# Optimization experiments

Measured on AMD Instinct MI355X. Metric: run time of the kernel, lower is better.

## Reference

```python
import jax, jax.numpy as jnp
import numpy as np

B, L, D_NODE, D_EDGE, H = 4, 256, 256, 128, 8
DK = D_NODE // H        # 32, per-head node dim
DE = D_EDGE // H        # 16, per-head edge dim
NEG_SLOPE = 0.2

# Static index maps replicating the torch loop indexing (including its j-1 off-by-one / wraparound bug)
_GIDX = np.arange(L - 1)[None, :] + (np.arange(L - 1)[None, :] >= np.arange(L)[:, None])  # [L, L-1]: j-values visited for row i (j != i, in order)
_PIDX = (np.arange(L) - 1) % (L - 1)   # [L]: torch uses attention_probs[:, j-1] for every j != i
_II = np.arange(L)[:, None]            # [L, 1]


def lrelu(x):
    return jnp.where(x >= 0, x, NEG_SLOPE * x)


def setup_inputs() -> dict:
    key = jax.random.key(0)
    ks = jax.random.split(key, 19)
    w = lambda k, s, sc=0.05: jax.random.normal(k, s, jnp.float32) * sc
    return dict(
        node=w(ks[0], (B, L, D_NODE), 1.0),
        edge=w(ks[1], (B, L, L, D_EDGE), 1.0),
        Wn_w=w(ks[2], (D_NODE, D_NODE)), Wn_b=w(ks[3], (D_NODE,)),
        Wh_w=w(ks[4], (DK, DK)), Wh_b=w(ks[5], (DK,)),
        We_w=w(ks[6], (D_EDGE, D_EDGE)), We_b=w(ks[7], (D_EDGE,)),
        Wn2_w=w(ks[8], (D_NODE, D_NODE)), Wn2_b=w(ks[9], (D_NODE,)),
        We2_w=w(ks[10], (D_EDGE, D_EDGE)), We2_b=w(ks[11], (D_EDGE,)),
        attn_w=w(ks[12], (2 * DK + DE,)),                  # attn_linear (no bias), input order [hi, hj, eij]
        edge_w=w(ks[13], (DE + 2 * DK, DE)), edge_b=w(ks[14], (DE,)),  # edge_linear, input order [eij, hi, hj]
        out_n_w=w(ks[15], (D_NODE, D_NODE)), out_n_b=w(ks[16], (D_NODE,)),
        out_e_w=w(ks[17], (D_EDGE, D_EDGE)), out_e_b=w(ks[18], (D_EDGE,)),
    )


def reference(node, edge, Wn_w, Wn_b, Wh_w, Wh_b, We_w, We_b, Wn2_w, Wn2_b,
              We2_w, We2_b, attn_w, edge_w, edge_b, out_n_w, out_n_b, out_e_w, out_e_b):
    node_p = (node @ Wn_w + Wn_b).reshape(B, L, H, DK)
    edge_p = (edge @ We_w + We_b).reshape(B, L, L, H, DE)

    # ---- node update (all heads at once) ----
    wq, wk, we = attn_w[:DK], attn_w[DK:2 * DK], attn_w[2 * DK:]
    si = jnp.einsum('bihd,d->bih', node_p, wq)
    sj = jnp.einsum('bjhd,d->bjh', node_p, wk)
    se = jnp.einsum('bijhd,d->bijh', edge_p, we)
    scores = si[:, :, None, :] + sj[:, None, :, :] + se          # [B,L,L,H], score(i,j)
    sc = scores[:, _II, _GIDX, :]                                 # [B,L,L-1,H]: j != i, loop order
    probs = jax.nn.softmax(lrelu(sc), axis=2)                     # softmax over the L-1 neighbors
    probs_pair = probs[:, :, _PIDX, :]                            # [B,L,L,H]: replicate probs[:, j-1]
    mask = (1.0 - jnp.eye(L, dtype=node.dtype))[None, :, :, None]
    Whh = jnp.einsum('bjhd,de->bjhe', node_p, Wh_w) + Wh_b        # Wh(hj), bias inside the sum
    agg = jnp.einsum('bijh,bjhe->bihe', probs_pair * mask, Whh)
    node_h = (node_p + lrelu(agg)).reshape(B, L, D_NODE)          # concat heads == reshape
    new_node = node_h @ out_n_w + out_n_b

    # ---- edge update ----
    node_p2 = (new_node @ Wn2_w + Wn2_b).reshape(B, L, H, DK)
    edge_p2 = (edge @ We2_w + We2_b).reshape(B, L, L, H, DE)
    w_e, w_i, w_j = edge_w[:DE], edge_w[DE:DE + DK], edge_w[DE + DK:]
    e_new = (jnp.einsum('bijhd,de->bijhe', edge_p2, w_e)
             + jnp.einsum('bihd,de->bihe', node_p2, w_i)[:, :, None]
             + jnp.einsum('bjhd,de->bjhe', node_p2, w_j)[:, None]
             + edge_b)
    e_new = e_new * mask[..., None]                               # diagonal stays zero (zeros_like init)
    new_edge = e_new.reshape(B, L, L, D_EDGE) @ out_e_w + out_e_b
    return new_node, new_edge
```

## Files before the change

### kernel.cpp

```cpp
#include <hip/hip_runtime.h>

#define Bb 4
#define Ll 256
#define NEG 0.2f

typedef __attribute__((ext_vector_type(8))) short short8;
typedef __attribute__((ext_vector_type(4))) float f32x4;
typedef __attribute__((ext_vector_type(4))) unsigned uint4v;

__device__ __forceinline__ float lrelu(float x) { return x >= 0.f ? x : NEG * x; }

__device__ __forceinline__ short f2bf(float x) {
  unsigned u = __builtin_bit_cast(unsigned, x);
  unsigned r = (u + 0x7FFFu + ((u >> 16) & 1u)) >> 16;
  return (short)r;
}

__device__ __forceinline__ unsigned pack2bf(float e, float o) {
  unsigned ue = __builtin_bit_cast(unsigned, e);
  unsigned uo = __builtin_bit_cast(unsigned, o);
  return ((ue + 0x8000u) >> 16) | ((uo + 0x8000u) & 0xFFFF0000u);
}

__device__ __forceinline__ float bflo(unsigned u) {
  return __builtin_bit_cast(float, u << 16);
}
__device__ __forceinline__ float bfhi(unsigned u) {
  return __builtin_bit_cast(float, u & 0xFFFF0000u);
}

__global__ void prep_kernel(const float* We_w, const float* We_b, const float* attn_w,
                            const float* We2_w, const float* We2_b, const float* edge_w,
                            const float* edge_b, const float* out_e_w, const float* out_e_b,
                            short* Vbf, float* chg, float* c0g, short* Gt) {
  int blk = blockIdx.x;
  int t = threadIdx.x;
  if (blk < 128) {
    __shared__ float m2[128];
    int c = blk;
    int h = t >> 4, e = t & 15;
    float s = 0.f;
    for (int d = 0; d < 16; ++d) s += We2_w[c * 128 + h * 16 + d] * edge_w[d * 16 + e];
    m2[t] = s;
    __syncthreads();
    float g = 0.f;
    for (int f = 0; f < 128; ++f) g += m2[f] * out_e_w[f * 128 + t];
    Gt[t * 128 + c] = f2bf(g);
  } else {
    __shared__ float b2e[128];
    const float* we = attn_w + 64;
    for (int idx = t; idx < 1024; idx += 128) {
      int c = idx >> 3, h = idx & 7;
      float s = 0.f;
      for (int d = 0; d < 16; ++d) s += We_w[c * 128 + h * 16 + d] * we[d];
      Vbf[h * 128 + c] = f2bf(s);
      Vbf[(h + 8) * 128 + c] = 0;
    }
    if (t < 8) {
      float s = 0.f;
      for (int d = 0; d < 16; ++d) s += We_b[t * 16 + d] * we[d];
      chg[t] = s;
    }
    {
      int h = t >> 4, e = t & 15;
      float s = 0.f;
      for (int d = 0; d < 16; ++d) s += We2_b[h * 16 + d] * edge_w[d * 16 + e];
      b2e[t] = s + edge_b[e];
    }
    __syncthreads();
    float s = out_e_b[t];
    for (int f = 0; f < 128; ++f) s += b2e[f] * out_e_w[f * 128 + t];
    c0g[t] = s;
  }
}

__global__ __launch_bounds__(256, 2) void edge_t_kernel(
    const float* __restrict__ edge, const short* __restrict__ Gt,
    const short* __restrict__ Vbf, const float* __restrict__ chg,
    short* __restrict__ Tf, float* __restrict__ seg) {
  int t = threadIdx.x;
  int l = t & 63, wid = t >> 6;
  int wm = wid >> 1, wn = wid & 1;
  int lc = l & 15, lq = l >> 4;
  long row0 = (long)blockIdx.x * 128;

  short8 bv[4][4];
#pragma unroll
  for (int ks = 0; ks < 4; ++ks)
#pragma unroll
    for (int nf = 0; nf < 4; ++nf)
      bv[ks][nf] = *(const short8*)(Gt + (wn * 64 + nf * 16 + lc) * 128 + ks * 32 + lq * 8);

  short8 vb[4];
#pragma unroll
  for (int ks = 0; ks < 4; ++ks) vb[ks] = *(const short8*)(Vbf + lc * 128 + ks * 32 + lq * 8);

  f32x4 accT[4][4];
#pragma unroll
  for (int mf = 0; mf < 4; ++mf)
#pragma unroll
    for (int nf = 0; nf < 4; ++nf) accT[mf][nf] = (f32x4){0.f, 0.f, 0.f, 0.f};
  f32x4 accS[4];
#pragma unroll
  for (int mf = 0; mf < 4; ++mf) accS[mf] = (f32x4){0.f, 0.f, 0.f, 0.f};

#pragma unroll
  for (int ks = 0; ks < 4; ++ks) {
    short8 av[4];
#pragma unroll
    for (int mf = 0; mf < 4; ++mf) {
      const float* ap = edge + (row0 + wm * 64 + mf * 16 + lc) * 128 + ks * 32 + lq * 8;
      float4 f0 = *(const float4*)ap;
      float4 f1 = *(const float4*)(ap + 4);
      uint4v u;
      u.x = pack2bf(f0.x, f0.y);
      u.y = pack2bf(f0.z, f0.w);
      u.z = pack2bf(f1.x, f1.y);
      u.w = pack2bf(f1.z, f1.w);
      av[mf] = __builtin_bit_cast(short8, u);
    }
#pragma unroll
    for (int mf = 0; mf < 4; ++mf)
#pragma unroll
      for (int nf = 0; nf < 4; ++nf)
        accT[mf][nf] =
            __builtin_amdgcn_mfma_f32_16x16x32_bf16(bv[ks][nf], av[mf], accT[mf][nf], 0, 0, 0);
    if (wn == 0) {
#pragma unroll
      for (int mf = 0; mf < 4; ++mf)
        accS[mf] = __builtin_amdgcn_mfma_f32_16x16x32_bf16(vb[ks], av[mf], accS[mf], 0, 0, 0);
    }
  }

  short* tb = Tf + (long)blockIdx.x * 16384;
#pragma unroll
  for (int mf = 0; mf < 4; ++mf)
#pragma unroll
    for (int np = 0; np < 2; ++np) {
      f32x4 a0 = accT[mf][2 * np];
      f32x4 a1 = accT[mf][2 * np + 1];
      uint4v u;
      u.x = pack2bf(a0.x, a0.y);
      u.y = pack2bf(a0.z, a0.w);
      u.z = pack2bf(a1.x, a1.y);
      u.w = pack2bf(a1.z, a1.w);
      *(uint4v*)(tb + (mf * 2 + np) * 2048 + t * 8) = u;
    }

  if (wn == 0 && lq < 2) {
    f32x4 chv = *(const f32x4*)(chg + lq * 4);
    long slab = blockIdx.x >> 1;
    int off = (blockIdx.x & 1) * 128;
#pragma unroll
    for (int mf = 0; mf < 4; ++mf) {
      int lrow = off + wm * 64 + mf * 16 + lc;
      f32x4 v = accS[mf] + chv;
      *(f32x4*)(seg + slab * 2048 + lrow * 8 + lq * 4) = v;
    }
  }
}

__global__ __launch_bounds__(256) void node_in_fused(
    const float* __restrict__ node, const float* __restrict__ Wn_w,
    const float* __restrict__ Wn_b, const float* __restrict__ Wh_w,
    const float* __restrict__ Wh_b, const float* __restrict__ attn_w,
    float* __restrict__ node_p, float* __restrict__ Whh, float* __restrict__ si,
    float* __restrict__ sj) {
  __shared__ float a[4][256];
  __shared__ float np[4][256];
  int t = threadIdx.x;
  int row0 = blockIdx.x * 4;
  for (int q = t; q < 1024; q += 256) a[q >> 8][q & 255] = node[(long)row0 * 256 + q];
  __syncthreads();
  float acc[4];
  float bvv = Wn_b[t];
#pragma unroll
  for (int r = 0; r < 4; ++r) acc[r] = bvv;
  for (int k = 0; k < 256; ++k) {
    float w = Wn_w[k * 256 + t];
#pragma unroll
    for (int r = 0; r < 4; ++r) acc[r] += a[r][k] * w;
  }
#pragma unroll
  for (int r = 0; r < 4; ++r) {
    node_p[(long)(row0 + r) * 256 + t] = acc[r];
    np[r][t] = acc[r];
  }
  __syncthreads();
  int h = t >> 5, e = t & 31;
  float wb2 = Wh_b[e];
#pragma unroll
  for (int r = 0; r < 4; ++r) {
    float s = wb2;
    for (int d = 0; d < 32; ++d) s += np[r][h * 32 + d] * Wh_w[d * 32 + e];
    Whh[(long)(row0 + r) * 256 + t] = s;
  }
  if (t < 64) {
    int r = t >> 4, idx = t & 15, hh = idx & 7;
    const float* w = attn_w + (idx < 8 ? 0 : 32);
    float s = 0.f;
    for (int d = 0; d < 32; ++d) s += np[r][hh * 32 + d] * w[d];
    ((idx < 8) ? si : sj)[(long)(row0 + r) * 8 + hh] = s;
  }
}

__global__ __launch_bounds__(256) void attn_fused(
    const float* __restrict__ node_p, const float* __restrict__ Whh,
    const float* __restrict__ si, const float* __restrict__ sj,
    const float* __restrict__ seg, float* __restrict__ node_h) {
  __shared__ float sjl[2048];
  __shared__ float sel[2048];
  __shared__ float pl[2048];
  __shared__ float sil[8];
  int t = threadIdx.x, bi = blockIdx.x;
  int b = bi >> 8, i = bi & 255;
  for (int q = t; q < 2048; q += 256) sjl[q] = sj[(long)b * 2048 + q];
  for (int q = t; q < 2048; q += 256) sel[q] = seg[(long)bi * 2048 + q];
  if (t < 8) sil[t] = si[(long)bi * 8 + t];
  __syncthreads();

  int g = t >> 5, l32 = t & 31;
  float sc[8];
  float mx = -1e30f;
#pragma unroll
  for (int m = 0; m < 8; ++m) {
    int k = l32 + 32 * m;
    float v = -1e30f;
    if (k < 255) {
      int jj = k + (k >= i ? 1 : 0);
      v = sil[g] + sjl[jj * 8 + g] + sel[jj * 8 + g];
      v = lrelu(v);
    }
    sc[m] = v;
    mx = fmaxf(mx, v);
  }
#pragma unroll
  for (int d = 16; d >= 1; d >>= 1) mx = fmaxf(mx, __shfl_xor(mx, d));
  float sum = 0.f;
#pragma unroll
  for (int m = 0; m < 8; ++m) {
    int k = l32 + 32 * m;
    float e = (k < 255) ? __expf(sc[m] - mx) : 0.f;
    sc[m] = e;
    sum += e;
  }
#pragma unroll
  for (int d = 16; d >= 1; d >>= 1) sum += __shfl_xor(sum, d);
  float inv = 1.f / sum;
#pragma unroll
  for (int m = 0; m < 8; ++m) {
    int k = l32 + 32 * m;
    if (k < 255) pl[k * 8 + g] = sc[m] * inv;
  }
  __syncthreads();

  int h = g;
  const float* wb = Whh + (long)b * 65536 + t;
  float acc0 = 0.f, acc1 = 0.f;
#pragma unroll 8
  for (int j = 0; j < 256; j += 2) {
    int k0 = (j == 0) ? 254 : (j - 1);
    int k1 = j;
    float w0 = (j == i) ? 0.f : pl[k0 * 8 + h];
    float w1 = (j + 1 == i) ? 0.f : pl[k1 * 8 + h];
    acc0 += w0 * wb[(long)j * 256];
    acc1 += w1 * wb[(long)(j + 1) * 256];
  }
  float acc = acc0 + acc1;
  float np = node_p[(long)bi * 256 + t];
  node_h[(long)bi * 256 + t] = np + lrelu(acc);
}

__global__ __launch_bounds__(256) void attn_fallback(
    const float* __restrict__ node_p, const float* __restrict__ Whh,
    const float* __restrict__ si, const float* __restrict__ sj,
    const float* __restrict__ edge, const short* __restrict__ Vbf,
    const float* __restrict__ chg, float* __restrict__ node_h) {
  __shared__ float sjl[2048];
  __shared__ float sel[2048];
  __shared__ float pl[2048];
  __shared__ float sil[8];
  int t = threadIdx.x, bi = blockIdx.x;
  int b = bi >> 8, i = bi & 255;
  for (int q = t; q < 2048; q += 256) sjl[q] = sj[(long)b * 2048 + q];
  if (t < 8) sil[t] = si[(long)bi * 8 + t];
  {
    int l = t & 63, w = t >> 6;
    int lc = l & 15, lq = l >> 4;
    short8 vb[4];
#pragma unroll
    for (int ks = 0; ks < 4; ++ks) vb[ks] = *(const short8*)(Vbf + lc * 128 + ks * 32 + lq * 8);
    f32x4 acc[4];
#pragma unroll
    for (int mf = 0; mf < 4; ++mf) acc[mf] = (f32x4){0.f, 0.f, 0.f, 0.f};
#pragma unroll
    for (int mf = 0; mf < 4; ++mf) {
      int row = w * 64 + mf * 16 + lc;
#pragma unroll
      for (int ks = 0; ks < 4; ++ks) {
        const float* ap = edge + (long)bi * 32768 + row * 128 + ks * 32 + lq * 8;
        float4 f0 = *(const float4*)ap;
        float4 f1 = *(const float4*)(ap + 4);
        uint4v u;
        u.x = pack2bf(f0.x, f0.y);
        u.y = pack2bf(f0.z, f0.w);
        u.z = pack2bf(f1.x, f1.y);
        u.w = pack2bf(f1.z, f1.w);
        acc[mf] = __builtin_amdgcn_mfma_f32_16x16x32_bf16(vb[ks], __builtin_bit_cast(short8, u),
                                                          acc[mf], 0, 0, 0);
      }
    }
    if (lq < 2) {
      f32x4 chv = *(const f32x4*)(chg + lq * 4);
#pragma unroll
      for (int mf = 0; mf < 4; ++mf) {
        int row = w * 64 + mf * 16 + lc;
        f32x4 v = acc[mf] + chv;
        *(f32x4*)(&sel[row * 8 + lq * 4]) = v;
      }
    }
  }
  __syncthreads();
  int g = t >> 5, l32 = t & 31;
  float sc[8];
  float mx = -1e30f;
#pragma unroll
  for (int m = 0; m < 8; ++m) {
    int k = l32 + 32 * m;
    float v = -1e30f;
    if (k < 255) {
      int jj = k + (k >= i ? 1 : 0);
      v = sil[g] + sjl[jj * 8 + g] + sel[jj * 8 + g];
      v = lrelu(v);
    }
    sc[m] = v;
    mx = fmaxf(mx, v);
  }
#pragma unroll
  for (int d = 16; d >= 1; d >>= 1) mx = fmaxf(mx, __shfl_xor(mx, d));
  float sum = 0.f;
#pragma unroll
  for (int m = 0; m < 8; ++m) {
    int k = l32 + 32 * m;
    float e = (k < 255) ? __expf(sc[m] - mx) : 0.f;
    sc[m] = e;
    sum += e;
  }
#pragma unroll
  for (int d = 16; d >= 1; d >>= 1) sum += __shfl_xor(sum, d);
  float inv = 1.f / sum;
#pragma unroll
  for (int m = 0; m < 8; ++m) {
    int k = l32 + 32 * m;
    if (k < 255) pl[k * 8 + g] = sc[m] * inv;
  }
  __syncthreads();
  int h = g;
  const float* wb = Whh + (long)b * 65536 + t;
  float acc0 = 0.f, acc1 = 0.f;
#pragma unroll 8
  for (int j = 0; j < 256; j += 2) {
    int k0 = (j == 0) ? 254 : (j - 1);
    int k1 = j;
    float w0 = (j == i) ? 0.f : pl[k0 * 8 + h];
    float w1 = (j + 1 == i) ? 0.f : pl[k1 * 8 + h];
    acc0 += w0 * wb[(long)j * 256];
    acc1 += w1 * wb[(long)(j + 1) * 256];
  }
  float acc = acc0 + acc1;
  float np = node_p[(long)bi * 256 + t];
  node_h[(long)bi * 256 + t] = np + lrelu(acc);
}

__global__ __launch_bounds__(256) void node_out_pq(
    const float* __restrict__ node_h, const float* __restrict__ out_n_w,
    const float* __restrict__ out_n_b, const float* __restrict__ Wn2_w,
    const float* __restrict__ Wn2_b, const float* __restrict__ edge_w,
    const float* __restrict__ out_e_w, float* __restrict__ out_node,
    float* __restrict__ Pg, float* __restrict__ Qg) {
  __shared__ float a[4][256];
  __shared__ float b2[4][256];
  __shared__ float ninj[4][256];
  int t = threadIdx.x;
  int row0 = blockIdx.x * 4;
  for (int q = t; q < 1024; q += 256) a[q >> 8][q & 255] = node_h[(long)row0 * 256 + q];
  __syncthreads();
  float acc[4];
  float bv1 = out_n_b[t];
#pragma unroll
  for (int r = 0; r < 4; ++r) acc[r] = bv1;
  for (int k = 0; k < 256; ++k) {
    float w = out_n_w[k * 256 + t];
#pragma unroll
    for (int r = 0; r < 4; ++r) acc[r] += a[r][k] * w;
  }
#pragma unroll
  for (int r = 0; r < 4; ++r) {
    out_node[(long)(row0 + r) * 256 + t] = acc[r];
    b2[r][t] = acc[r];
  }
  __syncthreads();
  float acc2[4];
  float bv2 = Wn2_b[t];
#pragma unroll
  for (int r = 0; r < 4; ++r) acc2[r] = bv2;
  for (int k = 0; k < 256; ++k) {
    float w = Wn2_w[k * 256 + t];
#pragma unroll
    for (int r = 0; r < 4; ++r) acc2[r] += b2[r][k] * w;
  }
#pragma unroll
  for (int r = 0; r < 4; ++r) a[r][t] = acc2[r];
  __syncthreads();
  {
    int f = t & 127, h = f >> 4, e = f & 15;
    const float* w = edge_w + 256 + (t >> 7) * 512;
#pragma unroll
    for (int r = 0; r < 4; ++r) {
      float s = 0.f;
      for (int d = 0; d < 32; ++d) s += a[r][h * 32 + d] * w[d * 16 + e];
      ninj[r][t] = s;
    }
  }
  __syncthreads();
  {
    int o = t & 127;
    int half = (t >> 7) * 128;
#pragma unroll
    for (int r = 0; r < 4; ++r) {
      float s = 0.f;
      const float* src = ninj[r] + half;
      for (int f = 0; f < 128; ++f) s += src[f] * out_e_w[f * 128 + o];
      ((t < 128) ? Pg : Qg)[(long)(row0 + r) * 128 + o] = s;
    }
  }
}

__global__ __launch_bounds__(256) void edge_final_kernel(
    const short* __restrict__ Tf, const float* __restrict__ Pg,
    const float* __restrict__ Qg, const float* __restrict__ c0g,
    const float* __restrict__ oeb, float* __restrict__ out_edge) {
  int t = threadIdx.x;
  int l = t & 63, wid = t >> 6;
  int wm = wid >> 1, wn = wid & 1;
  int lc = l & 15, lq = l >> 4;
  long row0 = (long)blockIdx.x * 128;
  int b = (int)(row0 >> 16);
  int i = (int)((row0 >> 8) & 255);
  int j0 = (int)(row0 & 255);

  const short* tb = Tf + (long)blockIdx.x * 16384;
  uint4v u[8];
#pragma unroll
  for (int q = 0; q < 8; ++q) u[q] = *(const uint4v*)(tb + q * 2048 + t * 8);

  f32x4 pc[4];
#pragma unroll
  for (int nf = 0; nf < 4; ++nf) {
    int cb = wn * 64 + nf * 16 + lq * 4;
    f32x4 p = *(const f32x4*)(Pg + ((long)(b * 256 + i)) * 128 + cb);
    f32x4 c0 = *(const f32x4*)(c0g + cb);
    pc[nf] = p + c0;
  }

#pragma unroll
  for (int mf = 0; mf < 4; ++mf) {
    int er = wm * 64 + mf * 16 + lc;
    int j = j0 + er;
    const float* Qrow = Qg + ((long)(b * 256 + j)) * 128;
    float* orow = out_edge + (row0 + er) * 128;
    if (j == i) {
#pragma unroll
      for (int nf = 0; nf < 4; ++nf) {
        int cb = wn * 64 + nf * 16 + lq * 4;
        *(f32x4*)(orow + cb) = *(const f32x4*)(oeb + cb);
      }
    } else {
#pragma unroll
      for (int np = 0; np < 2; ++np) {
        uint4v uu = u[mf * 2 + np];
        f32x4 v0 = {bflo(uu.x), bfhi(uu.x), bflo(uu.y), bfhi(uu.y)};
        f32x4 v1 = {bflo(uu.z), bfhi(uu.z), bflo(uu.w), bfhi(uu.w)};
        int nf0 = 2 * np, nf1 = 2 * np + 1;
        int cb0 = wn * 64 + nf0 * 16 + lq * 4;
        int cb1 = wn * 64 + nf1 * 16 + lq * 4;
        f32x4 q0 = *(const f32x4*)(Qrow + cb0);
        f32x4 q1 = *(const f32x4*)(Qrow + cb1);
        *(f32x4*)(orow + cb0) = v0 + pc[nf0] + q0;
        *(f32x4*)(orow + cb1) = v1 + pc[nf1] + q1;
      }
    }
  }
}

__global__ __launch_bounds__(256, 2) void edge_out_fallback(
    const float* __restrict__ edge, const short* __restrict__ Gt,
    const float* __restrict__ Pg, const float* __restrict__ Qg,
    const float* __restrict__ c0g, const float* __restrict__ oeb,
    float* __restrict__ out_edge) {
  int t = threadIdx.x;
  int l = t & 63, wid = t >> 6;
  int wm = wid >> 1, wn = wid & 1;
  int lc = l & 15, lq = l >> 4;
  long row0 = (long)blockIdx.x * 128;
  int b = (int)(row0 >> 16);
  int i = (int)((row0 >> 8) & 255);
  int j0 = (int)(row0 & 255);

  short8 bv[4][4];
#pragma unroll
  for (int ks = 0; ks < 4; ++ks)
#pragma unroll
    for (int nf = 0; nf < 4; ++nf)
      bv[ks][nf] = *(const short8*)(Gt + (wn * 64 + nf * 16 + lc) * 128 + ks * 32 + lq * 8);

  f32x4 acc[4][4];
#pragma unroll
  for (int mf = 0; mf < 4; ++mf)
#pragma unroll
    for (int nf = 0; nf < 4; ++nf) acc[mf][nf] = (f32x4){0.f, 0.f, 0.f, 0.f};

#pragma unroll
  for (int ks = 0; ks < 4; ++ks) {
    short8 av[4];
#pragma unroll
    for (int mf = 0; mf < 4; ++mf) {
      const float* ap = edge + (row0 + wm * 64 + mf * 16 + lc) * 128 + ks * 32 + lq * 8;
      float4 f0 = *(const float4*)ap;
      float4 f1 = *(const float4*)(ap + 4);
      uint4v u;
      u.x = pack2bf(f0.x, f0.y);
      u.y = pack2bf(f0.z, f0.w);
      u.z = pack2bf(f1.x, f1.y);
      u.w = pack2bf(f1.z, f1.w);
      av[mf] = __builtin_bit_cast(short8, u);
    }
#pragma unroll
    for (int mf = 0; mf < 4; ++mf)
#pragma unroll
      for (int nf = 0; nf < 4; ++nf)
        acc[mf][nf] =
            __builtin_amdgcn_mfma_f32_16x16x32_bf16(bv[ks][nf], av[mf], acc[mf][nf], 0, 0, 0);
  }

  f32x4 pc[4];
#pragma unroll
  for (int nf = 0; nf < 4; ++nf) {
    int cb = wn * 64 + nf * 16 + lq * 4;
    f32x4 p = *(const f32x4*)(Pg + ((long)(b * 256 + i)) * 128 + cb);
    f32x4 c0 = *(const f32x4*)(c0g + cb);
    pc[nf] = p + c0;
  }
#pragma unroll
  for (int mf = 0; mf < 4; ++mf) {
    int er = wm * 64 + mf * 16 + lc;
    int j = j0 + er;
    const float* Qrow = Qg + ((long)(b * 256 + j)) * 128;
    float* orow = out_edge + (row0 + er) * 128;
    if (j == i) {
#pragma unroll
      for (int nf = 0; nf < 4; ++nf) {
        int cb = wn * 64 + nf * 16 + lq * 4;
        *(f32x4*)(orow + cb) = *(const f32x4*)(oeb + cb);
      }
    } else {
#pragma unroll
      for (int nf = 0; nf < 4; ++nf) {
        int cb = wn * 64 + nf * 16 + lq * 4;
        f32x4 q4 = *(const f32x4*)(Qrow + cb);
        *(f32x4*)(orow + cb) = acc[mf][nf] + pc[nf] + q4;
      }
    }
  }
}

extern "C" void kernel_launch(void* const* d_in, const int* in_sizes, int n_in,
                              void* d_out, int out_size, void* d_ws, size_t ws_size,
                              hipStream_t stream) {
  const float* node = (const float*)d_in[0];
  const float* edge = (const float*)d_in[1];
  const float* Wn_w = (const float*)d_in[2];
  const float* Wn_b = (const float*)d_in[3];
  const float* Wh_w = (const float*)d_in[4];
  const float* Wh_b = (const float*)d_in[5];
  const float* We_w = (const float*)d_in[6];
  const float* We_b = (const float*)d_in[7];
  const float* Wn2_w = (const float*)d_in[8];
  const float* Wn2_b = (const float*)d_in[9];
  const float* We2_w = (const float*)d_in[10];
  const float* We2_b = (const float*)d_in[11];
  const float* attn_w = (const float*)d_in[12];
  const float* edge_w = (const float*)d_in[13];
  const float* edge_b = (const float*)d_in[14];
  const float* out_n_w = (const float*)d_in[15];
  const float* out_n_b = (const float*)d_in[16];
  const float* out_e_w = (const float*)d_in[17];
  const float* out_e_b = (const float*)d_in[18];

  float* out_node = (float*)d_out;
  float* out_edge = ((float*)d_out) + 262144;

  float* ws = (float*)d_ws;
  float* node_p = ws;
  float* Whh    = ws + 262144;
  float* node_h = ws + 524288;
  float* si     = ws + 786432;
  float* sjv    = ws + 794624;
  float* Pg     = ws + 802816;
  float* Qg     = ws + 933888;
  float* chg    = ws + 1064960;
  float* c0g    = ws + 1065088;
  short* Gt     = (short*)(ws + 1065216);
  short* Vbf    = (short*)(ws + 1073408);
  float* seg    = ws + 1074432;
  short* Tf     = (short*)(ws + 3171584);
  const bool big = ws_size >= (size_t)(3171584 + 16777216) * 4;

  prep_kernel<<<129, 128, 0, stream>>>(We_w, We_b, attn_w, We2_w, We2_b, edge_w, edge_b,
                                       out_e_w, out_e_b, Vbf, chg, c0g, Gt);
  node_in_fused<<<256, 256, 0, stream>>>(node, Wn_w, Wn_b, Wh_w, Wh_b, attn_w, node_p, Whh,
                                         si, sjv);
  if (big) {
    edge_t_kernel<<<2048, 256, 0, stream>>>(edge, Gt, Vbf, chg, Tf, seg);
    attn_fused<<<1024, 256, 0, stream>>>(node_p, Whh, si, sjv, seg, node_h);
    node_out_pq<<<256, 256, 0, stream>>>(node_h, out_n_w, out_n_b, Wn2_w, Wn2_b, edge_w,
                                         out_e_w, out_node, Pg, Qg);
    edge_final_kernel<<<2048, 256, 0, stream>>>(Tf, Pg, Qg, c0g, out_e_b, out_edge);
  } else {
    attn_fallback<<<1024, 256, 0, stream>>>(node_p, Whh, si, sjv, edge, Vbf, chg, node_h);
    node_out_pq<<<256, 256, 0, stream>>>(node_h, out_n_w, out_n_b, Wn2_w, Wn2_b, edge_w,
                                         out_e_w, out_node, Pg, Qg);
    edge_out_fallback<<<2048, 256, 0, stream>>>(edge, Gt, Pg, Qg, c0g, out_e_b, out_edge);
  }
}
```

Before: 177.3 us.

## Double-buffer edge tiles through LDS with async global-to-LDS loads in edge_t_kernel

Rewrites edge_t_kernel so each block walks 8 tiles of 32 edge rows, staging each next tile into a swizzled, double-buffered LDS buffer with global_load_lds while computing MFMAs on the current one. Per-wave accumulators shrink from 4x4 to 4 fragments, and the occupancy hint rises from 2 to 3 blocks per CU. The grid halves and the Tf intermediate layout changes to per-32-row tiles, with edge_final_kernel updated to read the new layout. The goal is to overlap the large edge-tensor read with compute, at the cost of a __syncthreads per tile and LDS usage that may limit occupancy.

```diff
diff --git a/kernel.cpp b/kernel.cpp
--- a/kernel.cpp
+++ b/kernel.cpp
@@ -74,15 +74,16 @@
   }
 }
 
-__global__ __launch_bounds__(256, 2) void edge_t_kernel(
+#define TPB_T 8
+__global__ __launch_bounds__(256, 3) void edge_t_kernel(
     const float* __restrict__ edge, const short* __restrict__ Gt,
     const short* __restrict__ Vbf, const float* __restrict__ chg,
     short* __restrict__ Tf, float* __restrict__ seg) {
+  __shared__ __align__(16) float abuf[2][32 * 128];
   int t = threadIdx.x;
   int l = t & 63, wid = t >> 6;
   int wm = wid >> 1, wn = wid & 1;
   int lc = l & 15, lq = l >> 4;
-  long row0 = (long)blockIdx.x * 128;
 
   short8 bv[4][4];
 #pragma unroll
@@ -90,73 +91,88 @@
 #pragma unroll
     for (int nf = 0; nf < 4; ++nf)
       bv[ks][nf] = *(const short8*)(Gt + (wn * 64 + nf * 16 + lc) * 128 + ks * 32 + lq * 8);
-
   short8 vb[4];
 #pragma unroll
   for (int ks = 0; ks < 4; ++ks) vb[ks] = *(const short8*)(Vbf + lc * 128 + ks * 32 + lq * 8);
 
-  f32x4 accT[4][4];
-#pragma unroll
-  for (int mf = 0; mf < 4; ++mf)
-#pragma unroll
-    for (int nf = 0; nf < 4; ++nf) accT[mf][nf] = (f32x4){0.f, 0.f, 0.f, 0.f};
-  f32x4 accS[4];
-#pragma unroll
-  for (int mf = 0; mf < 4; ++mf) accS[mf] = (f32x4){0.f, 0.f, 0.f, 0.f};
-
-#pragma unroll
-  for (int ks = 0; ks < 4; ++ks) {
-    short8 av[4];
-#pragma unroll
-    for (int mf = 0; mf < 4; ++mf) {
-      const float* ap = edge + (row0 + wm * 64 + mf * 16 + lc) * 128 + ks * 32 + lq * 8;
-      float4 f0 = *(const float4*)ap;
-      float4 f1 = *(const float4*)(ap + 4);
+  long tile0 = (long)blockIdx.x * TPB_T;
+  int wuni = (t >> 6);
+
+  auto stage = [&](int buf, long tile) {
+#pragma unroll
+    for (int q = 0; q < 4; ++q) {
+      int L = q * 256 + t;
+      int row = L >> 5, c4 = L & 31;
+      int scol = (c4 * 4) ^ ((row & 7) << 2);
+      const float* gp = edge + (tile * 32 + row) * 128 + scol;
+      char* lp = (char*)abuf[buf] + q * 4096 + wuni * 1024;
+      __builtin_amdgcn_global_load_lds(
+          (const __attribute__((address_space(1))) unsigned*)gp,
+          (__attribute__((address_space(3))) unsigned*)lp, 16, 0, 0);
+    }
+  };
+
+  stage(0, tile0);
+  __syncthreads();
+
+  int cur = 0;
+  for (int tt = 0; tt < TPB_T; ++tt) {
+    long tile = tile0 + tt;
+    if (tt + 1 < TPB_T) stage(cur ^ 1, tile + 1);
+
+    const char* base = (const char*)abuf[cur];
+    int row = wm * 16 + lc;
+    int sw = (row & 7) << 4;
+    const char* rbase = base + row * 512;
+
+    f32x4 accT[4];
+#pragma unroll
+    for (int nf = 0; nf < 4; ++nf) accT[nf] = (f32x4){0.f, 0.f, 0.f, 0.f};
+    f32x4 accS = (f32x4){0.f, 0.f, 0.f, 0.f};
+
+#pragma unroll
+    for (int ks = 0; ks < 4; ++ks) {
+      int cb = ks * 128 + lq * 32;
+      float4 f0 = *(const float4*)(rbase + (cb ^ sw));
+      float4 f1 = *(const float4*)(rbase + ((cb + 16) ^ sw));
       uint4v u;
       u.x = pack2bf(f0.x, f0.y);
       u.y = pack2bf(f0.z, f0.w);
       u.z = pack2bf(f1.x, f1.y);
       u.w = pack2bf(f1.z, f1.w);
-      av[mf] = __builtin_bit_cast(short8, u);
-    }
-#pragma unroll
-    for (int mf = 0; mf < 4; ++mf)
+      short8 av = __builtin_bit_cast(short8, u);
 #pragma unroll
       for (int nf = 0; nf < 4; ++nf)
-        accT[mf][nf] =
-            __builtin_amdgcn_mfma_f32_16x16x32_bf16(bv[ks][nf], av[mf], accT[mf][nf], 0, 0, 0);
-    if (wn == 0) {
-#pragma unroll
-      for (int mf = 0; mf < 4; ++mf)
-        accS[mf] = __builtin_amdgcn_mfma_f32_16x16x32_bf16(vb[ks], av[mf], accS[mf], 0, 0, 0);
-    }
-  }
-
-  short* tb = Tf + (long)blockIdx.x * 16384;
-#pragma unroll
-  for (int mf = 0; mf < 4; ++mf)
-#pragma unroll
-    for (int np = 0; np < 2; ++np) {
-      f32x4 a0 = accT[mf][2 * np];
-      f32x4 a1 = accT[mf][2 * np + 1];
-      uint4v u;
-      u.x = pack2bf(a0.x, a0.y);
-      u.y = pack2bf(a0.z, a0.w);
-      u.z = pack2bf(a1.x, a1.y);
-      u.w = pack2bf(a1.z, a1.w);
-      *(uint4v*)(tb + (mf * 2 + np) * 2048 + t * 8) = u;
-    }
-
-  if (wn == 0 && lq < 2) {
-    f32x4 chv = *(const f32x4*)(chg + lq * 4);
-    long slab = blockIdx.x >> 1;
-    int off = (blockIdx.x & 1) * 128;
-#pragma unroll
-    for (int mf = 0; mf < 4; ++mf) {
-      int lrow = off + wm * 64 + mf * 16 + lc;
-      f32x4 v = accS[mf] + chv;
+        accT[nf] = __builtin_amdgcn_mfma_f32_16x16x32_bf16(bv[ks][nf], av, accT[nf], 0, 0, 0);
+      if (wn == 0)
+        accS = __builtin_amdgcn_mfma_f32_16x16x32_bf16(vb[ks], av, accS, 0, 0, 0);
+    }
+
+    {
+      short* tb = Tf + tile * 4096 + wid * 1024 + l * 8;
+      uint4v u0, u1;
+      u0.x = pack2bf(accT[0].x, accT[0].y);
+      u0.y = pack2bf(accT[0].z, accT[0].w);
+      u0.z = pack2bf(accT[1].x, accT[1].y);
+      u0.w = pack2bf(accT[1].z, accT[1].w);
+      u1.x = pack2bf(accT[2].x, accT[2].y);
+      u1.y = pack2bf(accT[2].z, accT[2].w);
+      u1.z = pack2bf(accT[3].x, accT[3].y);
+      u1.w = pack2bf(accT[3].z, accT[3].w);
+      *(uint4v*)tb = u0;
+      *(uint4v*)(tb + 512) = u1;
+    }
+
+    if (wn == 0 && lq < 2) {
+      f32x4 chv = *(const f32x4*)(chg + lq * 4);
+      long slab = tile >> 3;
+      int lrow = (int)(tile & 7) * 32 + wm * 16 + lc;
+      f32x4 v = accS + chv;
       *(f32x4*)(seg + slab * 2048 + lrow * 8 + lq * 4) = v;
     }
+
+    __syncthreads();
+    cur ^= 1;
   }
 }
 
@@ -449,11 +465,6 @@
   int i = (int)((row0 >> 8) & 255);
   int j0 = (int)(row0 & 255);
 
-  const short* tb = Tf + (long)blockIdx.x * 16384;
-  uint4v u[8];
-#pragma unroll
-  for (int q = 0; q < 8; ++q) u[q] = *(const uint4v*)(tb + q * 2048 + t * 8);
-
   f32x4 pc[4];
 #pragma unroll
   for (int nf = 0; nf < 4; ++nf) {
@@ -464,8 +475,13 @@
   }
 
 #pragma unroll
-  for (int mf = 0; mf < 4; ++mf) {
-    int er = wm * 64 + mf * 16 + lc;
+  for (int st = 0; st < 4; ++st) {
+    long tile = blockIdx.x * 4 + st;
+    const short* tb = Tf + tile * 4096 + wid * 1024 + l * 8;
+    uint4v u0 = *(const uint4v*)tb;
+    uint4v u1 = *(const uint4v*)(tb + 512);
+
+    int er = st * 32 + wm * 16 + lc;
     int j = j0 + er;
     const float* Qrow = Qg + ((long)(b * 256 + j)) * 128;
     float* orow = out_edge + (row0 + er) * 128;
@@ -476,18 +492,16 @@
         *(f32x4*)(orow + cb) = *(const f32x4*)(oeb + cb);
       }
     } else {
-#pragma unroll
-      for (int np = 0; np < 2; ++np) {
-        uint4v uu = u[mf * 2 + np];
-        f32x4 v0 = {bflo(uu.x), bfhi(uu.x), bflo(uu.y), bfhi(uu.y)};
-        f32x4 v1 = {bflo(uu.z), bfhi(uu.z), bflo(uu.w), bfhi(uu.w)};
-        int nf0 = 2 * np, nf1 = 2 * np + 1;
-        int cb0 = wn * 64 + nf0 * 16 + lq * 4;
-        int cb1 = wn * 64 + nf1 * 16 + lq * 4;
-        f32x4 q0 = *(const f32x4*)(Qrow + cb0);
-        f32x4 q1 = *(const f32x4*)(Qrow + cb1);
-        *(f32x4*)(orow + cb0) = v0 + pc[nf0] + q0;
-        *(f32x4*)(orow + cb1) = v1 + pc[nf1] + q1;
+      f32x4 v[4];
+      v[0] = (f32x4){bflo(u0.x), bfhi(u0.x), bflo(u0.y), bfhi(u0.y)};
+      v[1] = (f32x4){bflo(u0.z), bfhi(u0.z), bflo(u0.w), bfhi(u0.w)};
+      v[2] = (f32x4){bflo(u1.x), bfhi(u1.x), bflo(u1.y), bfhi(u1.y)};
+      v[3] = (f32x4){bflo(u1.z), bfhi(u1.z), bflo(u1.w), bfhi(u1.w)};
+#pragma unroll
+      for (int nf = 0; nf < 4; ++nf) {
+        int cb = wn * 64 + nf * 16 + lq * 4;
+        f32x4 q4 = *(const f32x4*)(Qrow + cb);
+        *(f32x4*)(orow + cb) = v[nf] + pc[nf] + q4;
       }
     }
   }
@@ -621,7 +635,7 @@
   node_in_fused<<<256, 256, 0, stream>>>(node, Wn_w, Wn_b, Wh_w, Wh_b, attn_w, node_p, Whh,
                                          si, sjv);
   if (big) {
-    edge_t_kernel<<<2048, 256, 0, stream>>>(edge, Gt, Vbf, chg, Tf, seg);
+    edge_t_kernel<<<1024, 256, 0, stream>>>(edge, Gt, Vbf, chg, Tf, seg);
     attn_fused<<<1024, 256, 0, stream>>>(node_p, Whh, si, sjv, seg, node_h);
     node_out_pq<<<256, 256, 0, stream>>>(node_h, out_n_w, out_n_b, Wn2_w, Wn2_b, edge_w,
                                          out_e_w, out_node, Pg, Qg);
```

Measured after the change: 185.3 us. 4.5% more time.
